# Optimization experiments

Measured on AMD Instinct MI355X. Metric: run time of the kernel, lower is better.

## Reference

```python
import jax, jax.numpy as jnp
import numpy as np

# dims: StyleGAN2 modulated conv at 64x64, 512 channels
B, IC, OC, K, SD, H, W = 16, 512, 512, 3, 512, 64, 64
EPS = 1e-8


def setup_inputs() -> dict:
    key = jax.random.key(0)
    k1, k2, k3, k4 = jax.random.split(key, 4)
    return {
        "input": jax.random.normal(k1, (B, IC, H, W), dtype=jnp.float32),
        "style": jax.random.normal(k2, (B, SD), dtype=jnp.float32),
        # learned params
        "weight": jax.random.normal(k3, (1, OC, IC, K, K), dtype=jnp.float32),
        "mod_weight": jax.random.normal(k4, (IC, SD), dtype=jnp.float32),
        "mod_bias": jnp.ones((IC,), dtype=jnp.float32),  # bias_init=1
    }


def reference(input, style, weight, mod_weight, mod_bias):
    conv_scale = 1.0 / np.sqrt(IC * K * K)   # 1/sqrt(fan_in)
    mod_scale = 1.0 / np.sqrt(SD)            # EqualLinear scale, lr_mul=1

    # style modulation: EqualLinear(style_dim -> in_channel), no activation
    s = style @ (mod_weight * mod_scale).T + mod_bias          # [B, IC]

    # per-sample modulated weight [B, OC, IC, K, K]
    w = conv_scale * weight * s[:, None, :, None, None]
    # demodulation over (in_channel, kh, kw)
    demod = jax.lax.rsqrt(jnp.sum(w * w, axis=(2, 3, 4)) + EPS)  # [B, OC]
    w = w * demod[:, :, None, None, None]

    # grouped conv with groups=batch (same trick as torch F.conv2d groups=B)
    x = input.reshape(1, B * IC, H, W)
    wg = w.reshape(B * OC, IC, K, K)
    pad = K // 2
    out = jax.lax.conv_general_dilated(
        x, wg,
        window_strides=(1, 1),
        padding=[(pad, pad), (pad, pad)],
        dimension_numbers=("NCHW", "OIHW", "NCHW"),
        feature_group_count=B,
    )
    return out.reshape(B, OC, H, W)
```

## Files before the change

### kernel.cpp

```cpp
#include <hip/hip_runtime.h>
#include <hip/hip_bf16.h>

constexpr int BB = 16, IC = 512, OC = 512, HH = 64, WW = 64, HW = 64 * 64, SD = 512;
constexpr float MOD_SCALE = 0.04419417382415922f;
constexpr float CONV_SCALE = 0.014731391274719739f;
constexpr float CONV_SCALE2 = 2.170138888888889e-4f;

typedef float f32x4 __attribute__((ext_vector_type(4)));
typedef short bf16x8 __attribute__((ext_vector_type(8)));

#define VMWAIT(n) asm volatile("s_waitcnt vmcnt(" #n ")" ::: "memory")
#define LGKM0()   asm volatile("s_waitcnt lgkmcnt(0)" ::: "memory")

__device__ __forceinline__ unsigned short f2bf(float x) {
  __hip_bfloat16 h = __float2bfloat16(x);
  return *(unsigned short*)&h;
}

__global__ void k_style(const float* __restrict__ style, const float* __restrict__ mw,
                        const float* __restrict__ mb, float* __restrict__ s) {
  __shared__ float st[SD];
  const int b = blockIdx.x;
  for (int i = threadIdx.x; i < SD; i += 256) st[i] = style[b * SD + i];
  __syncthreads();
  for (int ic = threadIdx.x; ic < IC; ic += 256) {
    const float4* wr = (const float4*)(mw + (size_t)ic * SD);
    float acc = 0.f;
    for (int d = 0; d < SD / 4; ++d) {
      float4 w4 = wr[d];
      float4 s4 = *(const float4*)&st[d * 4];
      acc += w4.x * s4.x + w4.y * s4.y + w4.z * s4.z + w4.w * s4.w;
    }
    s[b * IC + ic] = acc * MOD_SCALE + mb[ic];
  }
}

__global__ void k_pack(const float* __restrict__ w, unsigned short* __restrict__ wpack,
                       float* __restrict__ w2sum) {
  const int oc = blockIdx.x;
  const int ic0 = threadIdx.x * 2;
  const float* p = w + (size_t)oc * IC * 9 + (size_t)ic0 * 9;
  float v[18];
#pragma unroll
  for (int i = 0; i < 18; ++i) v[i] = p[i];
  float s0 = 0.f, s1 = 0.f;
#pragma unroll
  for (int t = 0; t < 9; ++t) { s0 += v[t] * v[t]; s1 += v[9 + t] * v[9 + t]; }
  *(float2*)&w2sum[oc * IC + ic0] = make_float2(s0, s1);
#pragma unroll
  for (int t = 0; t < 9; ++t) {
    unsigned int pk = (unsigned int)f2bf(v[t]) | ((unsigned int)f2bf(v[9 + t]) << 16);
    *(unsigned int*)&wpack[((size_t)t * OC + oc) * IC + ic0] = pk;
  }
}

__global__ void k_demod(const float* __restrict__ s, const float* __restrict__ w2sum,
                        float* __restrict__ fscale) {
  __shared__ float s2[IC];
  const int b = blockIdx.x;
  for (int i = threadIdx.x; i < IC; i += 256) { float v = s[b * IC + i]; s2[i] = v * v; }
  __syncthreads();
  for (int oc = threadIdx.x; oc < OC; oc += 256) {
    const float4* wr = (const float4*)(w2sum + (size_t)oc * IC);
    float acc = 0.f;
    for (int i4 = 0; i4 < IC / 4; ++i4) {
      float4 w4 = wr[i4];
      float4 q4 = *(const float4*)&s2[i4 * 4];
      acc += w4.x * q4.x + w4.y * q4.y + w4.z * q4.z + w4.w * q4.w;
    }
    fscale[b * OC + oc] = CONV_SCALE * rsqrtf(CONV_SCALE2 * acc + 1e-8f);
  }
}

#define RD_AF(DST, NB)                                                         \
  do {                                                                         \
    _Pragma("unroll") for (int i_ = 0; i_ < 4; ++i_) {                         \
      int r_ = i_ * 16 + lrow;                                                 \
      DST[i_] = *(const bf16x8*)&Apw[(NB) * 2048 + r_ * 32 +                   \
                                     ((lk ^ ((r_ >> 1) & 3)) * 8)];            \
    }                                                                          \
  } while (0)

#define RD_BF(DST, TN, BSRC)                                                   \
  do {                                                                         \
    const int dh_ = (TN) / 3 - 1, dw_ = (TN) % 3 - 1;                          \
    _Pragma("unroll") for (int j_ = 0; j_ < 4; ++j_) {                         \
      int r_ = (wn + dh_ + 1) * 66 + j_ * 16 + lrow + dw_ + 1;                 \
      DST[j_] = *(const bf16x8*)&(BSRC)[r_ * 32 + ((lk ^ ((r_ >> 1) & 3)) * 8)];\
    }                                                                          \
  } while (0)

#define MFMA16(AF, BF)                                                         \
  do {                                                                         \
    _Pragma("unroll") for (int i_ = 0; i_ < 4; ++i_)                           \
      _Pragma("unroll") for (int j_ = 0; j_ < 4; ++j_)                         \
        acc[i_][j_] = __builtin_amdgcn_mfma_f32_16x16x32_bf16(AF[i_], BF[j_],  \
                                                              acc[i_][j_], 0, 0, 0); \
  } while (0)

__global__ __launch_bounds__(512, 2) void k_conv(
    const float* __restrict__ x, const unsigned short* __restrict__ wpack,
    const float* __restrict__ s, const float* __restrict__ fscale,
    float* __restrict__ out) {
  extern __shared__ __align__(128) unsigned short lds[];

  const int bx = ((blockIdx.x & 7) << 7) | (blockIdx.x >> 3);
  const int b = bx >> 6, mblk = (bx >> 5) & 1, nblk = bx & 31;

  const int tid = threadIdx.x;
  const int wave = tid >> 6, lane = tid & 63;
  const int wm = wave >> 1, wn = wave & 1;
  const int lrow = lane & 15, lk = lane >> 4;
  const int h0 = nblk * 2;

  unsigned short* Apw = lds + wave * 3 * 2048;
  unsigned short* Bsm0 = lds + 49152;
  unsigned short* Bsm1 = Bsm0 + 8448;

  const float* xb = x + (size_t)b * IC * HW;
  const float* sb = s + b * IC;

  f32x4 acc[4][4];
#pragma unroll
  for (int i = 0; i < 4; ++i)
#pragma unroll
    for (int j = 0; j < 4; ++j) acc[i][j] = f32x4{0.f, 0.f, 0.f, 0.f};

  {
    int q = tid >> 5;
    unsigned short* B = (q >> 3) ? Bsm1 : Bsm0;
    int hh = (q >> 1) & 3, wz = (q & 1) ? 65 : 0;
    B[(hh * 66 + wz) * 32 + (tid & 31)] = 0;
  }

  auto stageB = [&](int icb, unsigned short* dst) {
    const int hh = wave & 3;
    const int h_abs = h0 - 1 + hh;
    const bool vh = (h_abs >= 0) && (h_abs < HH);
    const int h_safe = vh ? h_abs : 0;
    const int r = hh * 66 + lane + 1;
    const int swz = (r >> 1) & 3;
    const float* src = xb + (size_t)(icb * 32) * HW + h_safe * WW + lane;
#pragma unroll
    for (int cc = 0; cc < 2; ++cc) {
      const int c = (wave >> 2) * 2 + cc;
      unsigned int pk[4];
#pragma unroll
      for (int jj = 0; jj < 4; ++jj) {
        int ic = c * 8 + jj * 2;
        float m0 = vh ? sb[icb * 32 + ic] : 0.f;
        float m1 = vh ? sb[icb * 32 + ic + 1] : 0.f;
        pk[jj] = (unsigned int)f2bf(src[(size_t)ic * HW] * m0) |
                 ((unsigned int)f2bf(src[(size_t)(ic + 1) * HW] * m1) << 16);
      }
      *(uint4*)&dst[r * 32 + ((c ^ swz) * 8)] = make_uint4(pk[0], pk[1], pk[2], pk[3]);
    }
  };

  auto issueA = [&](int tap, int icb, int nb) {
    const unsigned short* base =
        wpack + ((size_t)(tap * OC + mblk * 256 + wm * 64)) * IC + icb * 32;
    unsigned short* dst = Apw + nb * 2048;
#pragma unroll
    for (int q = 0; q < 4; ++q) {
      int rl = q * 16 + (lane >> 2);
      int cs = (lane & 3) ^ ((rl >> 1) & 3);
      const unsigned short* g = base + (size_t)rl * IC + cs * 8;
      __builtin_amdgcn_global_load_lds(
          (const __attribute__((address_space(1))) void*)g,
          (__attribute__((address_space(3))) void*)(dst + q * 16 * 32), 16, 0, 0);
    }
  };

  stageB(0, Bsm0);
  issueA(0, 0, 0);
  issueA(1, 0, 1);
  __syncthreads();

  bf16x8 afA[4], afB[4], bfA[4], bfB[4];
  RD_AF(afA, 0);
  RD_BF(bfA, 0, Bsm0);

  for (int e = 0; e < 16; e += 2) {
#pragma unroll
    for (int tt = 0; tt < 18; ++tt) {
      const int t = tt % 9;
      const int io = tt / 9;
      const int icb = e + io;
      const bool last = (e == 14) && (io == 1);
      const int P = (io + t) & 1;

      __builtin_amdgcn_s_barrier();
      __builtin_amdgcn_sched_barrier(0);

      __builtin_amdgcn_s_setprio(1);
      if (P == 0) { MFMA16(afA, bfA); } else { MFMA16(afB, bfB); }
      __builtin_amdgcn_s_setprio(0);
      __builtin_amdgcn_sched_barrier(0);

      if (!(last && t >= 7)) {
        if (t <= 6) issueA(t + 2, icb, (t + 2) % 3);
        else        issueA(t - 7, icb + 1, (t + 2) % 3);
      }

      if (!(last && t == 8)) {
        if (last && t == 7) { VMWAIT(0); } else { VMWAIT(4); }
        __builtin_amdgcn_sched_barrier(0);
        if (P == 0) {
          RD_AF(afB, (t + 1) % 3);
          if (t < 8) { RD_BF(bfB, t + 1, (io == 0 ? Bsm0 : Bsm1)); }
          else       { RD_BF(bfB, 0,     (io == 0 ? Bsm1 : Bsm0)); }
        } else {
          RD_AF(afA, (t + 1) % 3);
          if (t < 8) { RD_BF(bfA, t + 1, (io == 0 ? Bsm0 : Bsm1)); }
          else       { RD_BF(bfA, 0,     (io == 0 ? Bsm1 : Bsm0)); }
        }
      }

      if (t == 4 && !(e == 14 && io == 1)) {
        stageB(icb + 1, (io == 0 ? Bsm1 : Bsm0));
        LGKM0();
        __builtin_amdgcn_sched_barrier(0);
      }
    }
  }

  const float* fsb = fscale + b * OC;
#pragma unroll
  for (int i = 0; i < 4; ++i) {
#pragma unroll
    for (int rr = 0; rr < 4; ++rr) {
      const int oc = mblk * 256 + wm * 64 + i * 16 + lk * 4 + rr;
      const float sc = fsb[oc];
      float* orow = out + ((size_t)(b * OC + oc)) * HW + nblk * 128 + wn * 64 + lrow;
#pragma unroll
      for (int j = 0; j < 4; ++j) orow[j * 16] = acc[i][j][rr] * sc;
    }
  }
}

extern "C" void kernel_launch(void* const* d_in, const int* in_sizes, int n_in,
                              void* d_out, int out_size, void* d_ws, size_t ws_size,
                              hipStream_t stream) {
  const float* input = (const float*)d_in[0];
  const float* style = (const float*)d_in[1];
  const float* weight = (const float*)d_in[2];
  const float* mod_weight = (const float*)d_in[3];
  const float* mod_bias = (const float*)d_in[4];
  float* out = (float*)d_out;

  char* ws = (char*)d_ws;
  constexpr size_t WPACK_B = (size_t)9 * OC * IC * 2;
  constexpr size_t W2SUM_B = (size_t)OC * IC * 4;
  constexpr size_t S_B = (size_t)BB * IC * 4;
  unsigned short* wpack = (unsigned short*)ws;
  float* w2sum = (float*)(ws + WPACK_B);
  float* s = (float*)(ws + WPACK_B + W2SUM_B);
  float* fscale = (float*)(ws + WPACK_B + W2SUM_B + S_B);

  constexpr int LDS_BYTES = (8 * 3 * 2048 + 2 * 8448) * 2;
  hipFuncSetAttribute((const void*)k_conv,
                      hipFuncAttributeMaxDynamicSharedMemorySize, LDS_BYTES);

  k_style<<<BB, 256, 0, stream>>>(style, mod_weight, mod_bias, s);
  k_pack<<<OC, 256, 0, stream>>>(weight, wpack, w2sum);
  k_demod<<<BB, 256, 0, stream>>>(s, w2sum, fscale);
  k_conv<<<1024, 512, LDS_BYTES, stream>>>(input, wpack, s, fscale, out);
}
```

Baseline: 402.7 us.

## Halve conv block tile to 128 output channels with 256-thread blocks

The conv kernel now uses 4 waves per block covering 128 output channels instead of 8 waves covering 256. The grid doubles to 2048 blocks, and LDS moves to static arrays that are about half the size. Each block now stages the full input tile itself, so the bf16 conversion of the input and its global reads are done twice as often per output. In return, the kernel gets smaller blocks and more of them resident per CU.

Result: slower. 473.7 us (+17.6%).

```diff
diff --git a/kernel.cpp b/kernel.cpp
--- a/kernel.cpp
+++ b/kernel.cpp
@@ -76,17 +76,18 @@
   do {                                                                         \
     _Pragma("unroll") for (int i_ = 0; i_ < 4; ++i_) {                         \
       int r_ = i_ * 16 + lrow;                                                 \
-      DST[i_] = *(const bf16x8*)&Apw[(NB) * 2048 + r_ * 32 +                   \
-                                     ((lk ^ ((r_ >> 1) & 3)) * 8)];            \
+      DST[i_] = *(const bf16x8*)&Apool[wm][(NB)][r_ * 32 +                     \
+                                               ((lk ^ ((r_ >> 1) & 3)) * 8)];  \
     }                                                                          \
   } while (0)
 
-#define RD_BF(DST, TN, BSRC)                                                   \
+#define RD_BF(DST, TN, BI)                                                     \
   do {                                                                         \
     const int dh_ = (TN) / 3 - 1, dw_ = (TN) % 3 - 1;                          \
     _Pragma("unroll") for (int j_ = 0; j_ < 4; ++j_) {                         \
       int r_ = (wn + dh_ + 1) * 66 + j_ * 16 + lrow + dw_ + 1;                 \
-      DST[j_] = *(const bf16x8*)&(BSRC)[r_ * 32 + ((lk ^ ((r_ >> 1) & 3)) * 8)];\
+      DST[j_] = *(const bf16x8*)&Bsm[(BI)][r_ * 32 +                           \
+                                          ((lk ^ ((r_ >> 1) & 3)) * 8)];       \
     }                                                                          \
   } while (0)
 
@@ -98,14 +99,15 @@
                                                               acc[i_][j_], 0, 0, 0); \
   } while (0)
 
-__global__ __launch_bounds__(512, 2) void k_conv(
+__global__ __launch_bounds__(256, 2) void k_conv(
     const float* __restrict__ x, const unsigned short* __restrict__ wpack,
     const float* __restrict__ s, const float* __restrict__ fscale,
     float* __restrict__ out) {
-  extern __shared__ __align__(128) unsigned short lds[];
-
-  const int bx = ((blockIdx.x & 7) << 7) | (blockIdx.x >> 3);
-  const int b = bx >> 6, mblk = (bx >> 5) & 1, nblk = bx & 31;
+  __shared__ __align__(128) unsigned short Apool[2][3][64 * 32];
+  __shared__ __align__(128) unsigned short Bsm[2][264 * 32];
+
+  const int bx = ((blockIdx.x & 7) << 8) | (blockIdx.x >> 3);
+  const int b = bx >> 7, mblk = (bx >> 5) & 3, nblk = bx & 31;
 
   const int tid = threadIdx.x;
   const int wave = tid >> 6, lane = tid & 63;
@@ -113,10 +115,6 @@
   const int lrow = lane & 15, lk = lane >> 4;
   const int h0 = nblk * 2;
 
-  unsigned short* Apw = lds + wave * 3 * 2048;
-  unsigned short* Bsm0 = lds + 49152;
-  unsigned short* Bsm1 = Bsm0 + 8448;
-
   const float* xb = x + (size_t)b * IC * HW;
   const float* sb = s + b * IC;
 
@@ -126,15 +124,16 @@
 #pragma unroll
     for (int j = 0; j < 4; ++j) acc[i][j] = f32x4{0.f, 0.f, 0.f, 0.f};
 
-  {
-    int q = tid >> 5;
-    unsigned short* B = (q >> 3) ? Bsm1 : Bsm0;
+#pragma unroll
+  for (int z = 0; z < 2; ++z) {
+    int q = (tid >> 5) + z * 8;
+    int bi = q >> 3;
     int hh = (q >> 1) & 3, wz = (q & 1) ? 65 : 0;
-    B[(hh * 66 + wz) * 32 + (tid & 31)] = 0;
-  }
-
-  auto stageB = [&](int icb, unsigned short* dst) {
-    const int hh = wave & 3;
+    Bsm[bi][(hh * 66 + wz) * 32 + (tid & 31)] = 0;
+  }
+
+  auto stageB = [&](int icb, int bi) {
+    const int hh = wave;
     const int h_abs = h0 - 1 + hh;
     const bool vh = (h_abs >= 0) && (h_abs < HH);
     const int h_safe = vh ? h_abs : 0;
@@ -142,8 +141,7 @@
     const int swz = (r >> 1) & 3;
     const float* src = xb + (size_t)(icb * 32) * HW + h_safe * WW + lane;
 #pragma unroll
-    for (int cc = 0; cc < 2; ++cc) {
-      const int c = (wave >> 2) * 2 + cc;
+    for (int c = 0; c < 4; ++c) {
       unsigned int pk[4];
 #pragma unroll
       for (int jj = 0; jj < 4; ++jj) {
@@ -153,14 +151,14 @@
         pk[jj] = (unsigned int)f2bf(src[(size_t)ic * HW] * m0) |
                  ((unsigned int)f2bf(src[(size_t)(ic + 1) * HW] * m1) << 16);
       }
-      *(uint4*)&dst[r * 32 + ((c ^ swz) * 8)] = make_uint4(pk[0], pk[1], pk[2], pk[3]);
+      *(uint4*)&Bsm[bi][r * 32 + ((c ^ swz) * 8)] = make_uint4(pk[0], pk[1], pk[2], pk[3]);
     }
   };
 
   auto issueA = [&](int tap, int icb, int nb) {
     const unsigned short* base =
-        wpack + ((size_t)(tap * OC + mblk * 256 + wm * 64)) * IC + icb * 32;
-    unsigned short* dst = Apw + nb * 2048;
+        wpack + ((size_t)(tap * OC + mblk * 128 + wm * 64)) * IC + icb * 32;
+    unsigned short* dst = &Apool[wm][nb][0];
 #pragma unroll
     for (int q = 0; q < 4; ++q) {
       int rl = q * 16 + (lane >> 2);
@@ -172,14 +170,14 @@
     }
   };
 
-  stageB(0, Bsm0);
+  stageB(0, 0);
   issueA(0, 0, 0);
   issueA(1, 0, 1);
   __syncthreads();
 
   bf16x8 afA[4], afB[4], bfA[4], bfB[4];
   RD_AF(afA, 0);
-  RD_BF(bfA, 0, Bsm0);
+  RD_BF(bfA, 0, 0);
 
   for (int e = 0; e < 16; e += 2) {
 #pragma unroll
@@ -208,17 +206,17 @@
         __builtin_amdgcn_sched_barrier(0);
         if (P == 0) {
           RD_AF(afB, (t + 1) % 3);
-          if (t < 8) { RD_BF(bfB, t + 1, (io == 0 ? Bsm0 : Bsm1)); }
-          else       { RD_BF(bfB, 0,     (io == 0 ? Bsm1 : Bsm0)); }
+          if (t < 8) { RD_BF(bfB, t + 1, io); }
+          else       { RD_BF(bfB, 0, 1 - io); }
         } else {
           RD_AF(afA, (t + 1) % 3);
-          if (t < 8) { RD_BF(bfA, t + 1, (io == 0 ? Bsm0 : Bsm1)); }
-          else       { RD_BF(bfA, 0,     (io == 0 ? Bsm1 : Bsm0)); }
+          if (t < 8) { RD_BF(bfA, t + 1, io); }
+          else       { RD_BF(bfA, 0, 1 - io); }
         }
       }
 
       if (t == 4 && !(e == 14 && io == 1)) {
-        stageB(icb + 1, (io == 0 ? Bsm1 : Bsm0));
+        stageB(icb + 1, 1 - io);
         LGKM0();
         __builtin_amdgcn_sched_barrier(0);
       }
@@ -230,7 +228,7 @@
   for (int i = 0; i < 4; ++i) {
 #pragma unroll
     for (int rr = 0; rr < 4; ++rr) {
-      const int oc = mblk * 256 + wm * 64 + i * 16 + lk * 4 + rr;
+      const int oc = mblk * 128 + wm * 64 + i * 16 + lk * 4 + rr;
       const float sc = fsb[oc];
       float* orow = out + ((size_t)(b * OC + oc)) * HW + nblk * 128 + wn * 64 + lrow;
 #pragma unroll
@@ -258,12 +256,8 @@
   float* s = (float*)(ws + WPACK_B + W2SUM_B);
   float* fscale = (float*)(ws + WPACK_B + W2SUM_B + S_B);
 
-  constexpr int LDS_BYTES = (8 * 3 * 2048 + 2 * 8448) * 2;
-  hipFuncSetAttribute((const void*)k_conv,
-                      hipFuncAttributeMaxDynamicSharedMemorySize, LDS_BYTES);
-
   k_style<<<BB, 256, 0, stream>>>(style, mod_weight, mod_bias, s);
   k_pack<<<OC, 256, 0, stream>>>(weight, wpack, w2sum);
   k_demod<<<BB, 256, 0, stream>>>(s, w2sum, fscale);
-  k_conv<<<1024, 512, LDS_BYTES, stream>>>(input, wpack, s, fscale, out);
-}
+  k_conv<<<2048, 256, 0, stream>>>(input, wpack, s, fscale, out);
+}
```

## Shrink conv LDS footprint and raise occupancy target with shared A tiles

Applied to the files above, without the earlier changes.

The wn wave pairs now share one weight (A) staging buffer instead of each wave owning its own. The input (B) tile drops its padded halo columns, with out-of-range columns zeroed by clamping the address and selecting zero. The B-fragment register double buffer is removed: B fragments are now read from LDS right before each MFMA group rather than prefetched a step ahead. Launch bounds ask for 4 blocks per CU to gain occupancy, which caps registers hard and may cause spills, and the on-demand B reads expose LDS latency to the MFMAs.

After: 673.7 us. 1.67x slower.

```diff
diff --git a/kernel.cpp b/kernel.cpp
--- a/kernel.cpp
+++ b/kernel.cpp
@@ -81,12 +81,17 @@
     }                                                                          \
   } while (0)
 
-#define RD_BF(DST, TN, BSRC)                                                   \
+#define RD_BF(DST, TN, BP)                                                     \
   do {                                                                         \
     const int dh_ = (TN) / 3 - 1, dw_ = (TN) % 3 - 1;                          \
+    const int hb_ = wn + dh_ + 1;                                              \
     _Pragma("unroll") for (int j_ = 0; j_ < 4; ++j_) {                         \
-      int r_ = (wn + dh_ + 1) * 66 + j_ * 16 + lrow + dw_ + 1;                 \
-      DST[j_] = *(const bf16x8*)&(BSRC)[r_ * 32 + ((lk ^ ((r_ >> 1) & 3)) * 8)];\
+      int col_ = j_ * 16 + lrow + dw_;                                         \
+      int colc_ = col_ < 0 ? 0 : (col_ > 63 ? 63 : col_);                      \
+      int r_ = hb_ * 64 + colc_;                                               \
+      bf16x8 v_ = *(const bf16x8*)&(BP)[r_ * 32 + ((lk ^ ((r_ >> 1) & 3)) * 8)];\
+      bf16x8 z_ = {0, 0, 0, 0, 0, 0, 0, 0};                                    \
+      DST[j_] = (col_ == colc_) ? v_ : z_;                                     \
     }                                                                          \
   } while (0)
 
@@ -98,7 +103,7 @@
                                                               acc[i_][j_], 0, 0, 0); \
   } while (0)
 
-__global__ __launch_bounds__(512, 2) void k_conv(
+__global__ __launch_bounds__(512, 4) void k_conv(
     const float* __restrict__ x, const unsigned short* __restrict__ wpack,
     const float* __restrict__ s, const float* __restrict__ fscale,
     float* __restrict__ out) {
@@ -113,9 +118,9 @@
   const int lrow = lane & 15, lk = lane >> 4;
   const int h0 = nblk * 2;
 
-  unsigned short* Apw = lds + wave * 3 * 2048;
-  unsigned short* Bsm0 = lds + 49152;
-  unsigned short* Bsm1 = Bsm0 + 8448;
+  unsigned short* Apw = lds + wm * 3 * 2048;
+  unsigned short* Bsm0 = lds + 24576;
+  unsigned short* Bsm1 = Bsm0 + 8192;
 
   const float* xb = x + (size_t)b * IC * HW;
   const float* sb = s + b * IC;
@@ -125,20 +130,13 @@
   for (int i = 0; i < 4; ++i)
 #pragma unroll
     for (int j = 0; j < 4; ++j) acc[i][j] = f32x4{0.f, 0.f, 0.f, 0.f};
-
-  {
-    int q = tid >> 5;
-    unsigned short* B = (q >> 3) ? Bsm1 : Bsm0;
-    int hh = (q >> 1) & 3, wz = (q & 1) ? 65 : 0;
-    B[(hh * 66 + wz) * 32 + (tid & 31)] = 0;
-  }
 
   auto stageB = [&](int icb, unsigned short* dst) {
     const int hh = wave & 3;
     const int h_abs = h0 - 1 + hh;
     const bool vh = (h_abs >= 0) && (h_abs < HH);
     const int h_safe = vh ? h_abs : 0;
-    const int r = hh * 66 + lane + 1;
+    const int r = hh * 64 + lane;
     const int swz = (r >> 1) & 3;
     const float* src = xb + (size_t)(icb * 32) * HW + h_safe * WW + lane;
 #pragma unroll
@@ -177,9 +175,8 @@
   issueA(1, 0, 1);
   __syncthreads();
 
-  bf16x8 afA[4], afB[4], bfA[4], bfB[4];
+  bf16x8 afA[4], afB[4], bf[4];
   RD_AF(afA, 0);
-  RD_BF(bfA, 0, Bsm0);
 
   for (int e = 0; e < 16; e += 2) {
 #pragma unroll
@@ -193,8 +190,10 @@
       __builtin_amdgcn_s_barrier();
       __builtin_amdgcn_sched_barrier(0);
 
+      RD_BF(bf, t, (io == 0 ? Bsm0 : Bsm1));
+
       __builtin_amdgcn_s_setprio(1);
-      if (P == 0) { MFMA16(afA, bfA); } else { MFMA16(afB, bfB); }
+      if (P == 0) { MFMA16(afA, bf); } else { MFMA16(afB, bf); }
       __builtin_amdgcn_s_setprio(0);
       __builtin_amdgcn_sched_barrier(0);
 
@@ -206,15 +205,8 @@
       if (!(last && t == 8)) {
         if (last && t == 7) { VMWAIT(0); } else { VMWAIT(4); }
         __builtin_amdgcn_sched_barrier(0);
-        if (P == 0) {
-          RD_AF(afB, (t + 1) % 3);
-          if (t < 8) { RD_BF(bfB, t + 1, (io == 0 ? Bsm0 : Bsm1)); }
-          else       { RD_BF(bfB, 0,     (io == 0 ? Bsm1 : Bsm0)); }
-        } else {
-          RD_AF(afA, (t + 1) % 3);
-          if (t < 8) { RD_BF(bfA, t + 1, (io == 0 ? Bsm0 : Bsm1)); }
-          else       { RD_BF(bfA, 0,     (io == 0 ? Bsm1 : Bsm0)); }
-        }
+        if (P == 0) { RD_AF(afB, (t + 1) % 3); }
+        else        { RD_AF(afA, (t + 1) % 3); }
       }
 
       if (t == 4 && !(e == 14 && io == 1)) {
@@ -258,7 +250,7 @@
   float* s = (float*)(ws + WPACK_B + W2SUM_B);
   float* fscale = (float*)(ws + WPACK_B + W2SUM_B + S_B);
 
-  constexpr int LDS_BYTES = (8 * 3 * 2048 + 2 * 8448) * 2;
+  constexpr int LDS_BYTES = (4 * 3 * 2048 + 2 * 4 * 64 * 32) * 2;
   hipFuncSetAttribute((const void*)k_conv,
                       hipFuncAttributeMaxDynamicSharedMemorySize, LDS_BYTES);
 
```
